# Kernel optimization log

Hardware: AMD Instinct MI355X
Metric: run time of the kernel (lower is better)

## Reference

```python
import jax, jax.numpy as jnp
import numpy as np

DIM = 4096
NUM_EXPERTS = 8


def _simple_rmsnorm(x):
    # zeta SimpleRMSNorm: F.normalize(x, dim=-1) * sqrt(dim)
    n = jnp.linalg.norm(x, axis=-1, keepdims=True)
    return x / jnp.maximum(n, 1e-12) * (x.shape[-1] ** 0.5)


def _activation_quant(x):
    # per-token absmax int8 quant (BitNet 1.58)
    scale = 127.0 / jnp.clip(jnp.max(jnp.abs(x), axis=-1, keepdims=True), 1e-5, None)
    return jnp.clip(jnp.round(x * scale), -128, 127) / scale


def _weight_quant(w):
    # ternary weight quant with global mean-abs scale
    scale = 1.0 / jnp.clip(jnp.mean(jnp.abs(w)), 1e-5, None)
    return jnp.clip(jnp.round(w * scale), -1, 1) / scale


def setup_inputs() -> dict:
    key = jax.random.key(0)
    k1, k2, k3 = jax.random.split(key, 3)
    x = jax.random.normal(k1, (4, 4096, DIM), dtype=jnp.float32)
    # nn.Linear-style init scale
    W = jax.random.normal(k2, (NUM_EXPERTS, DIM), dtype=jnp.float32) * (DIM ** -0.5)
    b = jax.random.normal(k3, (NUM_EXPERTS,), dtype=jnp.float32) * 0.01
    return {"x": x, "W": W, "b": b}


def reference(x, W, b):
    xn = _simple_rmsnorm(x)                                   # [b, s, d]
    # straight-through quantization (forward = quantized value)
    xq = xn + jax.lax.stop_gradient(_activation_quant(xn) - xn)
    wq = W + jax.lax.stop_gradient(_weight_quant(W) - W)      # [e, d]
    logits = jnp.einsum("bsd,ed->bse", xq, wq) + b            # [b, s, e]
    return jax.nn.softmax(logits, axis=-1)
```

## Files before the change

### kernel.cpp

```cpp
#include <hip/hip_runtime.h>

#define DIM 4096
#define NE 8

#if __has_builtin(__builtin_amdgcn_sdot4)
__device__ __forceinline__ int dot4(int a, int b, int c) {
    return __builtin_amdgcn_sdot4(a, b, c, false);
}
#else
__device__ __forceinline__ int dot4(int a, int b, int c) {
    #pragma unroll
    for (int k = 0; k < 4; ++k)
        c += (int)(signed char)(a >> (8 * k)) * (int)(signed char)(b >> (8 * k));
    return c;
}
#endif

__device__ __forceinline__ unsigned pack4(int q0, int q1, int q2, int q3) {
    unsigned t0 = __builtin_amdgcn_perm((unsigned)q1, (unsigned)q0, 0x00000400u);
    unsigned t1 = __builtin_amdgcn_perm((unsigned)q3, (unsigned)q2, 0x00000400u);
    return __builtin_amdgcn_perm(t1, t0, 0x05040100u);
}

__global__ __launch_bounds__(1024) void wq_kernel(const float* __restrict__ W,
                                                  unsigned* __restrict__ wq32,
                                                  float* __restrict__ wscale) {
    __shared__ float red[16];
    const int tid = threadIdx.x, lane = tid & 63, wid = tid >> 6;

    const float4* W4 = (const float4*)W;
    float4 w[8];
    float s = 0.f;
    #pragma unroll
    for (int i = 0; i < 8; ++i) {
        w[i] = W4[i * 1024 + tid];
        s += fabsf(w[i].x) + fabsf(w[i].y) + fabsf(w[i].z) + fabsf(w[i].w);
    }
    #pragma unroll
    for (int o = 32; o > 0; o >>= 1) s += __shfl_xor(s, o, 64);
    if (lane == 0) red[wid] = s;
    __syncthreads();
    float tot = 0.f;
    #pragma unroll
    for (int k = 0; k < 16; ++k) tot += red[k];
    const float ws = 1.0f / fmaxf(tot * (1.0f / (NE * DIM)), 1e-5f);
    if (tid == 0) *wscale = ws;

    #pragma unroll
    for (int i = 0; i < 8; ++i) {
        const int idx = i * 1024 + tid;
        const int q0 = min(max((int)rintf(w[i].x * ws), -1), 1);
        const int q1 = min(max((int)rintf(w[i].y * ws), -1), 1);
        const int q2 = min(max((int)rintf(w[i].z * ws), -1), 1);
        const int q3 = min(max((int)rintf(w[i].w * ws), -1), 1);
        wq32[idx] = pack4(q0, q1, q2, q3);
    }
}

__global__ __launch_bounds__(256) void gate_kernel(const float* __restrict__ x,
                                                   const unsigned* __restrict__ wq32,
                                                   const float* __restrict__ wscale,
                                                   const float* __restrict__ bias,
                                                   float* __restrict__ out) {
    __shared__ float sred[4], ared[4];
    __shared__ int accred[4][NE];

    const int tid = threadIdx.x, lane = tid & 63, wid = tid >> 6;
    const size_t token = blockIdx.x;
    const float4* xrow = (const float4*)(x + token * (size_t)DIM);

    unsigned wreg[4][NE];
    #pragma unroll
    for (int r = 0; r < 4; ++r) {
        const int e4 = r * 256 + tid;
        #pragma unroll
        for (int e = 0; e < NE; ++e) wreg[r][e] = wq32[e * 1024 + e4];
    }

    float4 v[4];
    float ss = 0.f, amax = 0.f;
    #pragma unroll
    for (int r = 0; r < 4; ++r) {
        v[r] = xrow[r * 256 + tid];
        ss = fmaf(v[r].x, v[r].x, ss);
        ss = fmaf(v[r].y, v[r].y, ss);
        ss = fmaf(v[r].z, v[r].z, ss);
        ss = fmaf(v[r].w, v[r].w, ss);
        amax = fmaxf(amax, fmaxf(fmaxf(fabsf(v[r].x), fabsf(v[r].y)),
                                 fmaxf(fabsf(v[r].z), fabsf(v[r].w))));
    }
    #pragma unroll
    for (int o = 32; o > 0; o >>= 1) {
        ss  += __shfl_xor(ss, o, 64);
        amax = fmaxf(amax, __shfl_xor(amax, o, 64));
    }
    if (lane == 0) { sred[wid] = ss; ared[wid] = amax; }
    __syncthreads();
    ss   = sred[0] + sred[1] + sred[2] + sred[3];
    amax = fmaxf(fmaxf(ared[0], ared[1]), fmaxf(ared[2], ared[3]));

    const float n     = fmaxf(sqrtf(ss), 1e-12f);
    const float xnmax = (amax / n) * 64.0f;
    const float scale = 127.0f / fmaxf(xnmax, 1e-5f);
    const float m     = (64.0f / n) * scale;

    int acc[NE] = {0, 0, 0, 0, 0, 0, 0, 0};
    #pragma unroll
    for (int r = 0; r < 4; ++r) {
        const int q0 = (int)rintf(v[r].x * m);
        const int q1 = (int)rintf(v[r].y * m);
        const int q2 = (int)rintf(v[r].z * m);
        const int q3 = (int)rintf(v[r].w * m);
        const int packed = (int)pack4(q0, q1, q2, q3);
        #pragma unroll
        for (int e = 0; e < NE; ++e) acc[e] = dot4(packed, (int)wreg[r][e], acc[e]);
    }

    #pragma unroll
    for (int j = 0; j < 4; ++j) {
        const int give = (lane & 1) ? acc[2*j] : acc[2*j+1];
        const int got  = __shfl_xor(give, 1, 64);
        const int keep = (lane & 1) ? acc[2*j+1] : acc[2*j];
        acc[j] = keep + got;
    }
    #pragma unroll
    for (int j = 0; j < 2; ++j) {
        const int give = (lane & 2) ? acc[2*j] : acc[2*j+1];
        const int got  = __shfl_xor(give, 2, 64);
        const int keep = (lane & 2) ? acc[2*j+1] : acc[2*j];
        acc[j] = keep + got;
    }
    {
        const int give = (lane & 4) ? acc[0] : acc[1];
        const int got  = __shfl_xor(give, 4, 64);
        const int keep = (lane & 4) ? acc[1] : acc[0];
        acc[0] = keep + got;
    }
    #pragma unroll
    for (int o = 8; o < 64; o <<= 1) acc[0] += __shfl_xor(acc[0], o, 64);

    if (lane < NE) accred[wid][lane] = acc[0];
    __syncthreads();

    if (tid < NE) {
        const float inv = 1.0f / (scale * (*wscale));
        const int tot = accred[0][tid] + accred[1][tid] + accred[2][tid] + accred[3][tid];
        float logit = (float)tot * inv + bias[tid];
        float mx = logit;
        #pragma unroll
        for (int o = 1; o < NE; o <<= 1) mx = fmaxf(mx, __shfl_xor(mx, o, 64));
        const float p = expf(logit - mx);
        float s = p;
        #pragma unroll
        for (int o = 1; o < NE; o <<= 1) s += __shfl_xor(s, o, 64);
        out[token * NE + tid] = p / s;
    }
}

extern "C" void kernel_launch(void* const* d_in, const int* in_sizes, int n_in,
                              void* d_out, int out_size, void* d_ws, size_t ws_size,
                              hipStream_t stream) {
    const float* x = (const float*)d_in[0];
    const float* W = (const float*)d_in[1];
    const float* b = (const float*)d_in[2];
    float* out = (float*)d_out;

    unsigned* wq32   = (unsigned*)d_ws;
    float* wscale    = (float*)((char*)d_ws + 32768);

    const int tokens = in_sizes[0] / DIM;

    wq_kernel<<<1, 1024, 0, stream>>>(W, wq32, wscale);
    gate_kernel<<<tokens, 256, 0, stream>>>(x, wq32, wscale, b, out);
}
```

Before: 51.00 us.

## Map one token per wavefront and interleave packed ternary weights by expert

Each 64-lane wavefront now handles a whole token, so the block-level shared-memory reductions and both __syncthreads calls are removed, and each block processes four tokens. The weight quant kernel stores the packed weights interleaved as [group][expert], which lets each lane fetch all 8 experts' weights with two 16-byte loads that are prefetched one iteration ahead. In exchange each lane holds 16 float4 of activations in registers, which raises register pressure and may lower occupancy, and the launch assumes the token count is a multiple of 4.

```diff
diff --git a/kernel.cpp b/kernel.cpp
--- a/kernel.cpp
+++ b/kernel.cpp
@@ -49,11 +49,13 @@
     #pragma unroll
     for (int i = 0; i < 8; ++i) {
         const int idx = i * 1024 + tid;
+        const int e = idx >> 10;
+        const int g = idx & 1023;
         const int q0 = min(max((int)rintf(w[i].x * ws), -1), 1);
         const int q1 = min(max((int)rintf(w[i].y * ws), -1), 1);
         const int q2 = min(max((int)rintf(w[i].z * ws), -1), 1);
         const int q3 = min(max((int)rintf(w[i].w * ws), -1), 1);
-        wq32[idx] = pack4(q0, q1, q2, q3);
+        wq32[g * NE + e] = pack4(q0, q1, q2, q3);
     }
 }
 
@@ -62,26 +64,18 @@
                                                    const float* __restrict__ wscale,
                                                    const float* __restrict__ bias,
                                                    float* __restrict__ out) {
-    __shared__ float sred[4], ared[4];
-    __shared__ int accred[4][NE];
-
-    const int tid = threadIdx.x, lane = tid & 63, wid = tid >> 6;
-    const size_t token = blockIdx.x;
+    const int lane = threadIdx.x & 63;
+    const int wv   = threadIdx.x >> 6;
+    const size_t token = (size_t)blockIdx.x * 4 + wv;
     const float4* xrow = (const float4*)(x + token * (size_t)DIM);
 
-    unsigned wreg[4][NE];
+    float4 v[16];
     #pragma unroll
-    for (int r = 0; r < 4; ++r) {
-        const int e4 = r * 256 + tid;
-        #pragma unroll
-        for (int e = 0; e < NE; ++e) wreg[r][e] = wq32[e * 1024 + e4];
-    }
+    for (int r = 0; r < 16; ++r) v[r] = xrow[r * 64 + lane];
 
-    float4 v[4];
     float ss = 0.f, amax = 0.f;
     #pragma unroll
-    for (int r = 0; r < 4; ++r) {
-        v[r] = xrow[r * 256 + tid];
+    for (int r = 0; r < 16; ++r) {
         ss = fmaf(v[r].x, v[r].x, ss);
         ss = fmaf(v[r].y, v[r].y, ss);
         ss = fmaf(v[r].z, v[r].z, ss);
@@ -94,26 +88,37 @@
         ss  += __shfl_xor(ss, o, 64);
         amax = fmaxf(amax, __shfl_xor(amax, o, 64));
     }
-    if (lane == 0) { sred[wid] = ss; ared[wid] = amax; }
-    __syncthreads();
-    ss   = sred[0] + sred[1] + sred[2] + sred[3];
-    amax = fmaxf(fmaxf(ared[0], ared[1]), fmaxf(ared[2], ared[3]));
 
     const float n     = fmaxf(sqrtf(ss), 1e-12f);
     const float xnmax = (amax / n) * 64.0f;
     const float scale = 127.0f / fmaxf(xnmax, 1e-5f);
     const float m     = (64.0f / n) * scale;
 
+    const uint4* wp = (const uint4*)wq32;
     int acc[NE] = {0, 0, 0, 0, 0, 0, 0, 0};
+    uint4 wa = wp[(0 * 64 + lane) * 2 + 0];
+    uint4 wb = wp[(0 * 64 + lane) * 2 + 1];
     #pragma unroll
-    for (int r = 0; r < 4; ++r) {
+    for (int r = 0; r < 16; ++r) {
+        uint4 na, nb;
+        if (r < 15) {
+            na = wp[((r + 1) * 64 + lane) * 2 + 0];
+            nb = wp[((r + 1) * 64 + lane) * 2 + 1];
+        }
         const int q0 = (int)rintf(v[r].x * m);
         const int q1 = (int)rintf(v[r].y * m);
         const int q2 = (int)rintf(v[r].z * m);
         const int q3 = (int)rintf(v[r].w * m);
         const int packed = (int)pack4(q0, q1, q2, q3);
-        #pragma unroll
-        for (int e = 0; e < NE; ++e) acc[e] = dot4(packed, (int)wreg[r][e], acc[e]);
+        acc[0] = dot4(packed, (int)wa.x, acc[0]);
+        acc[1] = dot4(packed, (int)wa.y, acc[1]);
+        acc[2] = dot4(packed, (int)wa.z, acc[2]);
+        acc[3] = dot4(packed, (int)wa.w, acc[3]);
+        acc[4] = dot4(packed, (int)wb.x, acc[4]);
+        acc[5] = dot4(packed, (int)wb.y, acc[5]);
+        acc[6] = dot4(packed, (int)wb.z, acc[6]);
+        acc[7] = dot4(packed, (int)wb.w, acc[7]);
+        wa = na; wb = nb;
     }
 
     #pragma unroll
@@ -139,13 +144,9 @@
     #pragma unroll
     for (int o = 8; o < 64; o <<= 1) acc[0] += __shfl_xor(acc[0], o, 64);
 
-    if (lane < NE) accred[wid][lane] = acc[0];
-    __syncthreads();
-
-    if (tid < NE) {
+    if (lane < NE) {
         const float inv = 1.0f / (scale * (*wscale));
-        const int tot = accred[0][tid] + accred[1][tid] + accred[2][tid] + accred[3][tid];
-        float logit = (float)tot * inv + bias[tid];
+        float logit = (float)acc[0] * inv + bias[lane];
         float mx = logit;
         #pragma unroll
         for (int o = 1; o < NE; o <<= 1) mx = fmaxf(mx, __shfl_xor(mx, o, 64));
@@ -153,7 +154,7 @@
         float s = p;
         #pragma unroll
         for (int o = 1; o < NE; o <<= 1) s += __shfl_xor(s, o, 64);
-        out[token * NE + tid] = p / s;
+        out[token * NE + lane] = p / s;
     }
 }
 
@@ -171,5 +172,5 @@
     const int tokens = in_sizes[0] / DIM;
 
     wq_kernel<<<1, 1024, 0, stream>>>(W, wq32, wscale);
-    gate_kernel<<<tokens, 256, 0, stream>>>(x, wq32, wscale, b, out);
+    gate_kernel<<<tokens / 4, 256, 0, stream>>>(x, wq32, wscale, b, out);
 }
```

Result: slower. 55.19 us (+8.2%).
